# Optimization experiments

Hardware: AMD Instinct MI355X
Metric: run time of the kernel (lower is better)

Reference implementation:

```python
import jax, jax.numpy as jnp
import numpy as np

D_MODEL = 2048
NUM_HEADS = 32
NUM_GROUPS = 8
D_K = D_MODEL // NUM_HEADS          # 64
HPG = NUM_HEADS // NUM_GROUPS       # heads per group = 4
B, S = 2, 2048


def setup_inputs() -> dict:
    key = jax.random.key(0)
    ks = jax.random.split(key, 9)
    w_scale = 0.02
    kv_dim = NUM_GROUPS * D_K
    return {
        "x":  jax.random.normal(ks[0], (B, S, D_MODEL), dtype=jnp.float32),
        "Wq": jax.random.normal(ks[1], (D_MODEL, D_MODEL), dtype=jnp.float32) * w_scale,
        "bq": jnp.zeros((D_MODEL,), dtype=jnp.float32),
        "Wk": jax.random.normal(ks[2], (D_MODEL, kv_dim), dtype=jnp.float32) * w_scale,
        "bk": jnp.zeros((kv_dim,), dtype=jnp.float32),
        "Wv": jax.random.normal(ks[3], (D_MODEL, kv_dim), dtype=jnp.float32) * w_scale,
        "bv": jnp.zeros((kv_dim,), dtype=jnp.float32),
        "Wo": jax.random.normal(ks[4], (D_MODEL, D_MODEL), dtype=jnp.float32) * w_scale,
        "bo": jnp.zeros((D_MODEL,), dtype=jnp.float32),
    }


def reference(x, Wq, bq, Wk, bk, Wv, bv, Wo, bo):
    b, s, _ = x.shape
    # projections (torch Linear math: x @ W^T + b, here weights stored as (in,out))
    Q = (x @ Wq + bq).reshape(b, s, NUM_HEADS, D_K).transpose(0, 2, 1, 3)   # [B,H,S,dk]
    Kg = (x @ Wk + bk).reshape(b, s, NUM_GROUPS, D_K).transpose(0, 2, 1, 3)  # [B,G,S,dk]
    Vg = (x @ Wv + bv).reshape(b, s, NUM_GROUPS, D_K).transpose(0, 2, 1, 3)
    # repeat_interleave K/V over head dim to full head count
    K = jnp.repeat(Kg, HPG, axis=1)  # [B,H,S,dk]
    V = jnp.repeat(Vg, HPG, axis=1)
    scores = jnp.einsum("bhqd,bhkd->bhqk", Q, K) / np.sqrt(D_K).astype(np.float32)
    attn = jax.nn.softmax(scores, axis=-1)
    out = jnp.einsum("bhqk,bhkd->bhqd", attn, V)               # [B,H,S,dk]
    out = out.transpose(0, 2, 1, 3).reshape(b, s, D_MODEL)
    out = out @ Wo + bo
    # module returns grouped K,V cache: K[:, ::HPG] == Kg
    return out, (Kg, Vg)
```

## Files before the change

kernel.cpp:

```cpp
#include <hip/hip_runtime.h>
#include <hip/hip_bf16.h>
#include <stdint.h>

#define S_LEN 2048
#define DM    2048
#define NH    32
#define NG    8
#define DK    64
#define BATCH 2
#define MROWS (BATCH*S_LEN)
#define NQKV  3072
#define SSCALE 0.18033688f

typedef __bf16 bf16x8 __attribute__((ext_vector_type(8)));
typedef short  s16x8  __attribute__((ext_vector_type(8)));
typedef float  f32x4  __attribute__((ext_vector_type(4)));
typedef unsigned int u32x4 __attribute__((ext_vector_type(4)));

__device__ __forceinline__ unsigned short f2b(float f) {
    unsigned int x = __float_as_uint(f);
    unsigned int r = (x + 0x7fffu + ((x >> 16) & 1u)) >> 16;
    return (unsigned short)r;
}
__device__ __forceinline__ bf16x8 ld8(const unsigned short* p) {
    return *(const bf16x8*)p;
}
__device__ __forceinline__ s16x8 cvt8(const float* p) {
    f32x4 a = *(const f32x4*)p;
    f32x4 b = *(const f32x4*)(p + 4);
    s16x8 o;
#pragma unroll
    for (int j = 0; j < 4; j++) { o[j] = (short)f2b(a[j]); o[4 + j] = (short)f2b(b[j]); }
    return o;
}
__device__ __forceinline__ void gl_lds(const unsigned short* g, unsigned short* l) {
    __builtin_amdgcn_global_load_lds(
        (const __attribute__((address_space(1))) unsigned int*)g,
        (__attribute__((address_space(3))) unsigned int*)l, 16, 0, 0);
}
__device__ __forceinline__ void wait_vm4() {
    asm volatile("s_waitcnt vmcnt(4)" ::: "memory");
}
__device__ __forceinline__ void wait_vm0() {
    asm volatile("s_waitcnt vmcnt(0)" ::: "memory");
}
__device__ __forceinline__ void bar() {
    __builtin_amdgcn_sched_barrier(0);
    __builtin_amdgcn_s_barrier();
    __builtin_amdgcn_sched_barrier(0);
}

#define TCVT 4096
#define TQ   4096
#define TK   1024
#define TV   1024
#define TO   4096
#define TB   12
#define NPREP (TCVT+TQ+TK+TV+TO+TB)
__global__ __launch_bounds__(256) void prep_fused(
    const float* __restrict__ x,
    const float* __restrict__ Wq, const float* __restrict__ Wk,
    const float* __restrict__ Wv, const float* __restrict__ Wo,
    const float* __restrict__ bq, const float* __restrict__ bk,
    const float* __restrict__ bv,
    unsigned short* __restrict__ xb,
    unsigned short* __restrict__ WqkvT, unsigned short* __restrict__ WoT,
    float* __restrict__ bqkv) {
    __shared__ float t[32][33];
    int bid = blockIdx.x;
    const int tx = threadIdx.x, ty = threadIdx.y;
    const int flat = ty * 32 + tx;
    if (bid < TCVT) {
        size_t id = (size_t)bid * 256 + flat;
        *(s16x8*)&xb[id * 8] = cvt8(x + id * 8);
        return;
    }
    bid -= TCVT;
    const float* in; unsigned short* out; int C, bx, by;
    if (bid < TQ) { in = Wq; out = WqkvT; C = DM; bx = bid & 63; by = bid >> 6; }
    else if ((bid -= TQ) < TK) { in = Wk; out = WqkvT + (size_t)2048 * DM; C = 512; bx = bid & 15; by = bid >> 4; }
    else if ((bid -= TK) < TV) { in = Wv; out = WqkvT + (size_t)2560 * DM; C = 512; bx = bid & 15; by = bid >> 4; }
    else if ((bid -= TV) < TO) { in = Wo; out = WoT; C = DM; bx = bid & 63; by = bid >> 6; }
    else {
        int i = (bid - TO) * 256 + flat;
        if (i < 2048) bqkv[i] = bq[i];
        else if (i < 2560) bqkv[i] = bk[i - 2048];
        else if (i < 3072) bqkv[i] = bv[i - 2560];
        return;
    }
    const int R = DM;
    int c0 = bx * 32, r0 = by * 32;
#pragma unroll
    for (int i = 0; i < 4; i++)
        t[ty + i * 8][tx] = in[(size_t)(r0 + ty + i * 8) * C + c0 + tx];
    __syncthreads();
#pragma unroll
    for (int i = 0; i < 4; i++)
        out[(size_t)(c0 + ty + i * 8) * R + r0 + tx] = f2b(t[tx][ty + i * 8]);
}

__device__ __forceinline__ void xcd_remap(int gx, int* bx, int* by) {
    int nwg = gx * (int)gridDim.y;
    int flat = (int)blockIdx.y * gx + (int)blockIdx.x;
    int wgid = (flat & 7) * (nwg >> 3) + (flat >> 3);
    *bx = wgid % gx;
    *by = wgid / gx;
}

__global__ __launch_bounds__(256, 3) void gemm_qkv(const unsigned short* __restrict__ A,
                                                const unsigned short* __restrict__ Bt,
                                                const float* __restrict__ bias,
                                                unsigned short* __restrict__ Qb,
                                                float* __restrict__ Kg, float* __restrict__ Vg,
                                                unsigned short* __restrict__ Kb,
                                                unsigned short* __restrict__ Vtb) {
    __shared__ alignas(16) unsigned short As[3][128 * 32];
    __shared__ alignas(16) unsigned short Bs[3][128 * 32];
    const int K = DM;
    const int tid = threadIdx.x;
    int bx, by;
    xcd_remap(NQKV / 128, &bx, &by);
    const int n0 = bx * 128, m0 = by * 128;
    const int w = tid >> 6, lane = tid & 63;
    const int ln15 = lane & 15, quad = lane >> 4;
    const int wm = (w >> 1) * 64, wn = (w & 1) * 64;
    const int xq = (quad ^ ((ln15 >> 1) & 3)) * 8;
    f32x4 acc[4][4] = {};

#define GSTAGE(k0v, buf) do {                                                    \
    _Pragma("unroll")                                                            \
    for (int i = 0; i < 2; ++i) {                                                \
        int s = w * 128 + i * 64 + lane;             \
        int r = s >> 2, cb = (s & 3) ^ ((r >> 1) & 3);                           \
        gl_lds(&A[(size_t)(m0 + r) * K + (k0v) + cb * 8],                        \
               &As[buf][(w * 128 + i * 64) * 8]);                                \
        gl_lds(&Bt[(size_t)(n0 + r) * K + (k0v) + cb * 8],                       \
               &Bs[buf][(w * 128 + i * 64) * 8]);                                \
    } } while (0)

    GSTAGE(0, 0);
    GSTAGE(32, 1);
    int cur = 0;
    for (int k0 = 0; k0 < K; k0 += 32) {
        if (k0 + 32 < K) wait_vm4(); else wait_vm0();
        bar();
        if (k0 + 64 < K) {
            int nb = cur + 2; if (nb >= 3) nb -= 3;
            GSTAGE(k0 + 64, nb);
        }
        bf16x8 af[4], bfr[4];
#pragma unroll
        for (int mt = 0; mt < 4; mt++)
            af[mt] = ld8(&As[cur][(wm + mt * 16 + ln15) * 32 + xq]);
#pragma unroll
        for (int nt = 0; nt < 4; nt++)
            bfr[nt] = ld8(&Bs[cur][(wn + nt * 16 + ln15) * 32 + xq]);
        __builtin_amdgcn_s_setprio(1);
#pragma unroll
        for (int mt = 0; mt < 4; mt++)
#pragma unroll
            for (int nt = 0; nt < 4; nt++)
                acc[mt][nt] = __builtin_amdgcn_mfma_f32_16x16x32_bf16(af[mt], bfr[nt], acc[mt][nt], 0, 0, 0);
        __builtin_amdgcn_s_setprio(0);
        cur = (cur + 1 == 3) ? 0 : cur + 1;
    }
#undef GSTAGE
#pragma unroll
    for (int nt = 0; nt < 4; nt++) {
        int col = n0 + wn + nt * 16 + ln15;
        float bv = bias[col];
#pragma unroll
        for (int mt = 0; mt < 4; mt++) {
            int row0 = m0 + wm + mt * 16 + quad * 4;
#pragma unroll
            for (int r = 0; r < 4; r++) {
                float val = acc[mt][nt][r] + bv;
                int row = row0 + r;
                int b = row >> 11, s = row & 2047;
                if (col < 2048) {
                    Qb[(size_t)row * DM + col] = f2b(val * SSCALE);
                } else if (col < 2560) {
                    int gc = col - 2048, g = gc >> 6, d = gc & 63;
                    size_t idx = (((size_t)(b * NG + g) * S_LEN + s) << 6) + d;
                    Kg[idx] = val;
                    Kb[idx] = f2b(val);
                } else {
                    int gc = col - 2560, g = gc >> 6, d = gc & 63;
                    Vg[(((size_t)(b * NG + g) * S_LEN + s) << 6) + d] = val;
                    Vtb[((size_t)(b * NG + g) * DK + d) * S_LEN + s] = f2b(val);
                }
            }
        }
    }
}

__global__ __launch_bounds__(256, 3) void gemm_o(const unsigned short* __restrict__ A,
                                              const unsigned short* __restrict__ Bt,
                                              const float* __restrict__ bias,
                                              float* __restrict__ C) {
    __shared__ alignas(16) unsigned short As[3][128 * 32];
    __shared__ alignas(16) unsigned short Bs[3][128 * 32];
    const int K = DM, N = DM;
    const int tid = threadIdx.x;
    int bx, by;
    xcd_remap(DM / 128, &bx, &by);
    const int n0 = bx * 128, m0 = by * 128;
    const int w = tid >> 6, lane = tid & 63;
    const int ln15 = lane & 15, quad = lane >> 4;
    const int wm = (w >> 1) * 64, wn = (w & 1) * 64;
    const int xq = (quad ^ ((ln15 >> 1) & 3)) * 8;
    f32x4 acc[4][4] = {};

#define GSTAGE(k0v, buf) do {                                                    \
    _Pragma("unroll")                                                            \
    for (int i = 0; i < 2; ++i) {                                                \
        int s = w * 128 + i * 64 + lane;                                         \
        int r = s >> 2, cb = (s & 3) ^ ((r >> 1) & 3);                           \
        gl_lds(&A[(size_t)(m0 + r) * K + (k0v) + cb * 8],                        \
               &As[buf][(w * 128 + i * 64) * 8]);                                \
        gl_lds(&Bt[(size_t)(n0 + r) * K + (k0v) + cb * 8],                       \
               &Bs[buf][(w * 128 + i * 64) * 8]);                                \
    } } while (0)

    GSTAGE(0, 0);
    GSTAGE(32, 1);
    int cur = 0;
    for (int k0 = 0; k0 < K; k0 += 32) {
        if (k0 + 32 < K) wait_vm4(); else wait_vm0();
        bar();
        if (k0 + 64 < K) {
            int nb = cur + 2; if (nb >= 3) nb -= 3;
            GSTAGE(k0 + 64, nb);
        }
        bf16x8 af[4], bfr[4];
#pragma unroll
        for (int mt = 0; mt < 4; mt++)
            af[mt] = ld8(&As[cur][(wm + mt * 16 + ln15) * 32 + xq]);
#pragma unroll
        for (int nt = 0; nt < 4; nt++)
            bfr[nt] = ld8(&Bs[cur][(wn + nt * 16 + ln15) * 32 + xq]);
        __builtin_amdgcn_s_setprio(1);
#pragma unroll
        for (int mt = 0; mt < 4; mt++)
#pragma unroll
            for (int nt = 0; nt < 4; nt++)
                acc[mt][nt] = __builtin_amdgcn_mfma_f32_16x16x32_bf16(af[mt], bfr[nt], acc[mt][nt], 0, 0, 0);
        __builtin_amdgcn_s_setprio(0);
        cur = (cur + 1 == 3) ? 0 : cur + 1;
    }
#undef GSTAGE
#pragma unroll
    for (int nt = 0; nt < 4; nt++) {
        int col = n0 + wn + nt * 16 + ln15;
        float bv = bias[col];
#pragma unroll
        for (int mt = 0; mt < 4; mt++) {
            int row0 = m0 + wm + mt * 16 + quad * 4;
#pragma unroll
            for (int r = 0; r < 4; r++)
                C[(size_t)(row0 + r) * N + col] = acc[mt][nt][r] + bv;
        }
    }
}

#define MT 2
__global__ __launch_bounds__(512, 4) void attn_fwd(const unsigned short* __restrict__ Qb,
                                                   const unsigned short* __restrict__ Kb,
                                                   const unsigned short* __restrict__ Vtb,
                                                   unsigned short* __restrict__ AO) {
    __shared__ alignas(16) unsigned short Ks[2][2][64 * 64];
    __shared__ alignas(16) unsigned short Vt[2][2][64 * 64];
    const int b = blockIdx.z, h = blockIdx.y, q0 = blockIdx.x * 256;
    const int g = h >> 2;
    const int tid = threadIdx.x;
    const int w = tid >> 6, lane = tid & 63;
    const int ln15 = lane & 15, quad = lane >> 4;
    const int x7a = (quad ^ (ln15 & 7)) * 8;
    const int x7b = x7a ^ 32;

    bf16x8 aq[MT][2];
#pragma unroll
    for (int mt = 0; mt < MT; mt++) {
        const size_t qrow =
            ((size_t)(b * S_LEN + q0 + w * 32 + mt * 16 + ln15)) * DM + h * DK;
        aq[mt][0] = ld8(&Qb[qrow + quad * 8]);
        aq[mt][1] = ld8(&Qb[qrow + 32 + quad * 8]);
    }

    bf16x8 ones;
#pragma unroll
    for (int j = 0; j < 8; j++) ones[j] = (__bf16)1.0f;

    f32x4 o[MT][4] = {};
    f32x4 l_acc[MT] = {};
    const size_t kvb = ((size_t)(b * NG + g)) * S_LEN * DK;

#define STAGE(k0v, buf) do {                                                     \
    int r = tid >> 3, cb = (tid & 7) ^ (r & 7);                                  \
    _Pragma("unroll")                                                            \
    for (int j = 0; j < 2; j++) {                                                \
        gl_lds(&Kb[kvb + (size_t)((k0v) + j * 64 + r) * DK + cb * 8],            \
               &Ks[buf][j][(w * 64) * 8]);                                       \
        gl_lds(&Vtb[kvb + (size_t)r * S_LEN + (k0v) + j * 64 + cb * 8],          \
               &Vt[buf][j][(w * 64) * 8]);                                       \
    } } while (0)

    STAGE(0, 0);
    wait_vm0();
    __syncthreads();
    int cur = 0;

    for (int k0 = 0; k0 < S_LEN; k0 += 128) {
        if (k0 + 128 < S_LEN) STAGE(k0 + 128, cur ^ 1);

#pragma unroll
        for (int sub = 0; sub < 2; sub++) {
            f32x4 z[MT][4];
            __builtin_amdgcn_s_setprio(1);
#pragma unroll
            for (int nt = 0; nt < 4; nt++) {
                bf16x8 bk0 = ld8(&Ks[cur][sub][(nt * 16 + ln15) * 64 + x7a]);
                bf16x8 bk1 = ld8(&Ks[cur][sub][(nt * 16 + ln15) * 64 + x7b]);
#pragma unroll
                for (int mt = 0; mt < MT; mt++) {
                    f32x4 t = {0.f, 0.f, 0.f, 0.f};
                    t = __builtin_amdgcn_mfma_f32_16x16x32_bf16(bk0, aq[mt][0], t, 0, 0, 0);
                    t = __builtin_amdgcn_mfma_f32_16x16x32_bf16(bk1, aq[mt][1], t, 0, 0, 0);
                    z[mt][nt] = t;
                }
            }
            __builtin_amdgcn_s_setprio(0);

            bf16x8 pa[MT][2];
#pragma unroll
            for (int mt = 0; mt < MT; mt++) {
                unsigned int S[4][2];
#pragma unroll
                for (int nt = 0; nt < 4; nt++) {
                    f32x4 pe;
#pragma unroll
                    for (int r = 0; r < 4; r++)
                        pe[r] = __builtin_amdgcn_exp2f(z[mt][nt][r]);
                    asm("v_cvt_pk_bf16_f32 %0, %1, %2" : "=v"(S[nt][0]) : "v"(pe[0]), "v"(pe[1]));
                    asm("v_cvt_pk_bf16_f32 %0, %1, %2" : "=v"(S[nt][1]) : "v"(pe[2]), "v"(pe[3]));
                }
#pragma unroll
                for (int f = 0; f < 2; f++) {
                    unsigned int wA[2], wB[2];
#pragma unroll
                    for (int p = 0; p < 2; p++) {
                        unsigned int xa = S[2 * f][p], yb = S[2 * f + 1][p];
                        asm("v_permlane32_swap_b32 %0, %1" : "+v"(xa), "+v"(yb));
                        asm("v_permlane16_swap_b32 %0, %1" : "+v"(xa), "+v"(yb));
                        wA[p] = xa; wB[p] = yb;
                    }
                    u32x4 t4;
                    t4[0] = wA[0]; t4[1] = wA[1]; t4[2] = wB[0]; t4[3] = wB[1];
                    pa[mt][f] = __builtin_bit_cast(bf16x8, t4);
                }
            }

            __builtin_amdgcn_s_setprio(1);
#pragma unroll
            for (int nt = 0; nt < 4; nt++) {
                bf16x8 bv0 = ld8(&Vt[cur][sub][(nt * 16 + ln15) * 64 + x7a]);
                bf16x8 bv1 = ld8(&Vt[cur][sub][(nt * 16 + ln15) * 64 + x7b]);
#pragma unroll
                for (int mt = 0; mt < MT; mt++) {
                    f32x4 t = o[mt][nt];
                    t = __builtin_amdgcn_mfma_f32_16x16x32_bf16(pa[mt][0], bv0, t, 0, 0, 0);
                    t = __builtin_amdgcn_mfma_f32_16x16x32_bf16(pa[mt][1], bv1, t, 0, 0, 0);
                    o[mt][nt] = t;
                }
            }
#pragma unroll
            for (int mt = 0; mt < MT; mt++) {
                l_acc[mt] = __builtin_amdgcn_mfma_f32_16x16x32_bf16(pa[mt][0], ones, l_acc[mt], 0, 0, 0);
                l_acc[mt] = __builtin_amdgcn_mfma_f32_16x16x32_bf16(pa[mt][1], ones, l_acc[mt], 0, 0, 0);
            }
            __builtin_amdgcn_s_setprio(0);
        }

        wait_vm0();
        __syncthreads();
        cur ^= 1;
    }
#undef STAGE

#pragma unroll
    for (int mt = 0; mt < MT; mt++) {
#pragma unroll
        for (int r = 0; r < 4; r++) {
            float inv = 1.0f / l_acc[mt][r];
            int q = q0 + w * 32 + mt * 16 + quad * 4 + r;
#pragma unroll
            for (int nt = 0; nt < 4; nt++) {
                int col = h * DK + nt * 16 + ln15;
                *(__bf16*)&AO[((size_t)(b * S_LEN + q)) * DM + col] =
                    (__bf16)(o[mt][nt][r] * inv);
            }
        }
    }
}

extern "C" void kernel_launch(void* const* d_in, const int* in_sizes, int n_in,
                              void* d_out, int out_size, void* d_ws, size_t ws_size,
                              hipStream_t stream) {
    const float* x  = (const float*)d_in[0];
    const float* Wq = (const float*)d_in[1];
    const float* bq = (const float*)d_in[2];
    const float* Wk = (const float*)d_in[3];
    const float* bk = (const float*)d_in[4];
    const float* Wv = (const float*)d_in[5];
    const float* bv = (const float*)d_in[6];
    const float* Wo = (const float*)d_in[7];
    const float* bo = (const float*)d_in[8];

    float* out = (float*)d_out;
    float* Kg  = out + (size_t)MROWS * DM;
    float* Vg  = Kg + (size_t)BATCH * NG * S_LEN * DK;

    unsigned short* Qb = (unsigned short*)d_out;

    unsigned short* ws    = (unsigned short*)d_ws;
    unsigned short* WqkvT = ws;
    unsigned short* WoT   = WqkvT + (size_t)NQKV * DM;
    unsigned short* Kb    = WoT + (size_t)DM * DM;
    unsigned short* Vtb   = Kb + (size_t)BATCH * NG * S_LEN * DK;
    unsigned short* AO    = Vtb + (size_t)BATCH * NG * S_LEN * DK;
    unsigned short* xb    = AO + (size_t)MROWS * DM;
    float*          bqkv  = (float*)(xb + (size_t)MROWS * DM);

    hipLaunchKernelGGL(prep_fused, dim3(NPREP), dim3(32, 8), 0, stream,
                       x, Wq, Wk, Wv, Wo, bq, bk, bv, xb, WqkvT, WoT, bqkv);

    hipLaunchKernelGGL(gemm_qkv, dim3(NQKV / 128, MROWS / 128), dim3(256), 0, stream,
                       xb, WqkvT, bqkv, Qb, Kg, Vg, Kb, Vtb);

    hipLaunchKernelGGL(attn_fwd, dim3(S_LEN / 256, NH, BATCH), dim3(512), 0, stream,
                       Qb, Kb, Vtb, AO);

    hipLaunchKernelGGL(gemm_o, dim3(DM / 128, MROWS / 128), dim3(256), 0, stream,
                       AO, WoT, bo, out);
}
```

Baseline: 305.4 us.

## Use 64-row transpose tiles in prep and double-buffer BK=64 in output GEMM

```diff
diff --git a/kernel.cpp b/kernel.cpp
--- a/kernel.cpp
+++ b/kernel.cpp
@@ -51,10 +51,10 @@
 }
 
 #define TCVT 4096
-#define TQ   4096
-#define TK   1024
-#define TV   1024
-#define TO   4096
+#define TQ   2048
+#define TK   512
+#define TV   512
+#define TO   2048
 #define TB   12
 #define NPREP (TCVT+TQ+TK+TV+TO+TB)
 __global__ __launch_bounds__(256) void prep_fused(
@@ -66,7 +66,7 @@
     unsigned short* __restrict__ xb,
     unsigned short* __restrict__ WqkvT, unsigned short* __restrict__ WoT,
     float* __restrict__ bqkv) {
-    __shared__ float t[32][33];
+    __shared__ float t[32][65];
     int bid = blockIdx.x;
     const int tx = threadIdx.x, ty = threadIdx.y;
     const int flat = ty * 32 + tx;
@@ -88,15 +88,15 @@
         else if (i < 3072) bqkv[i] = bv[i - 2560];
         return;
     }
-    const int R = DM;
-    int c0 = bx * 32, r0 = by * 32;
-#pragma unroll
-    for (int i = 0; i < 4; i++)
-        t[ty + i * 8][tx] = in[(size_t)(r0 + ty + i * 8) * C + c0 + tx];
+    int c0 = bx * 32, r0 = by * 64;
+#pragma unroll
+    for (int i = 0; i < 8; i++)
+        t[tx][ty + i * 8] = in[(size_t)(r0 + ty + i * 8) * C + c0 + tx];
     __syncthreads();
-#pragma unroll
-    for (int i = 0; i < 4; i++)
-        out[(size_t)(c0 + ty + i * 8) * R + r0 + tx] = f2b(t[tx][ty + i * 8]);
+    const int rt = flat & 63, cg = flat >> 6;
+#pragma unroll
+    for (int i = 0; i < 8; i++)
+        out[(size_t)(c0 + cg * 8 + i) * DM + r0 + rt] = f2b(t[cg * 8 + i][rt]);
 }
 
 __device__ __forceinline__ void xcd_remap(int gx, int* bx, int* by) {
@@ -194,12 +194,12 @@
     }
 }
 
-__global__ __launch_bounds__(256, 3) void gemm_o(const unsigned short* __restrict__ A,
+__global__ __launch_bounds__(256, 2) void gemm_o(const unsigned short* __restrict__ A,
                                               const unsigned short* __restrict__ Bt,
                                               const float* __restrict__ bias,
                                               float* __restrict__ C) {
-    __shared__ alignas(16) unsigned short As[3][128 * 32];
-    __shared__ alignas(16) unsigned short Bs[3][128 * 32];
+    __shared__ alignas(16) unsigned short As[2][2][128 * 32];
+    __shared__ alignas(16) unsigned short Bs[2][2][128 * 32];
     const int K = DM, N = DM;
     const int tid = threadIdx.x;
     int bx, by;
@@ -211,44 +211,48 @@
     const int xq = (quad ^ ((ln15 >> 1) & 3)) * 8;
     f32x4 acc[4][4] = {};
 
-#define GSTAGE(k0v, buf) do {                                                    \
+#define GSTAGE64(k0v, buf) do {                                                  \
     _Pragma("unroll")                                                            \
-    for (int i = 0; i < 2; ++i) {                                                \
-        int s = w * 128 + i * 64 + lane;                                         \
-        int r = s >> 2, cb = (s & 3) ^ ((r >> 1) & 3);                           \
-        gl_lds(&A[(size_t)(m0 + r) * K + (k0v) + cb * 8],                        \
-               &As[buf][(w * 128 + i * 64) * 8]);                                \
-        gl_lds(&Bt[(size_t)(n0 + r) * K + (k0v) + cb * 8],                       \
-               &Bs[buf][(w * 128 + i * 64) * 8]);                                \
+    for (int j = 0; j < 2; ++j) {                                                \
+        _Pragma("unroll")                                                        \
+        for (int i = 0; i < 2; ++i) {                                            \
+            int s = w * 128 + i * 64 + lane;                                     \
+            int r = s >> 2, cb = (s & 3) ^ ((r >> 1) & 3);                       \
+            gl_lds(&A[(size_t)(m0 + r) * K + (k0v) + j * 32 + cb * 8],           \
+                   &As[buf][j][(w * 128 + i * 64) * 8]);                         \
+            gl_lds(&Bt[(size_t)(n0 + r) * K + (k0v) + j * 32 + cb * 8],          \
+                   &Bs[buf][j][(w * 128 + i * 64) * 8]);                         \
+        }                                                                        \
     } } while (0)
 
-    GSTAGE(0, 0);
-    GSTAGE(32, 1);
+    GSTAGE64(0, 0);
+    wait_vm0();
+    __syncthreads();
     int cur = 0;
-    for (int k0 = 0; k0 < K; k0 += 32) {
-        if (k0 + 32 < K) wait_vm4(); else wait_vm0();
-        bar();
-        if (k0 + 64 < K) {
-            int nb = cur + 2; if (nb >= 3) nb -= 3;
-            GSTAGE(k0 + 64, nb);
-        }
-        bf16x8 af[4], bfr[4];
-#pragma unroll
-        for (int mt = 0; mt < 4; mt++)
-            af[mt] = ld8(&As[cur][(wm + mt * 16 + ln15) * 32 + xq]);
-#pragma unroll
-        for (int nt = 0; nt < 4; nt++)
-            bfr[nt] = ld8(&Bs[cur][(wn + nt * 16 + ln15) * 32 + xq]);
-        __builtin_amdgcn_s_setprio(1);
-#pragma unroll
-        for (int mt = 0; mt < 4; mt++)
+    for (int k0 = 0; k0 < K; k0 += 64) {
+        if (k0 + 64 < K) GSTAGE64(k0 + 64, cur ^ 1);
+#pragma unroll
+        for (int sub = 0; sub < 2; sub++) {
+            bf16x8 af[4], bfr[4];
+#pragma unroll
+            for (int mt = 0; mt < 4; mt++)
+                af[mt] = ld8(&As[cur][sub][(wm + mt * 16 + ln15) * 32 + xq]);
 #pragma unroll
             for (int nt = 0; nt < 4; nt++)
-                acc[mt][nt] = __builtin_amdgcn_mfma_f32_16x16x32_bf16(af[mt], bfr[nt], acc[mt][nt], 0, 0, 0);
-        __builtin_amdgcn_s_setprio(0);
-        cur = (cur + 1 == 3) ? 0 : cur + 1;
-    }
-#undef GSTAGE
+                bfr[nt] = ld8(&Bs[cur][sub][(wn + nt * 16 + ln15) * 32 + xq]);
+            __builtin_amdgcn_s_setprio(1);
+#pragma unroll
+            for (int mt = 0; mt < 4; mt++)
+#pragma unroll
+                for (int nt = 0; nt < 4; nt++)
+                    acc[mt][nt] = __builtin_amdgcn_mfma_f32_16x16x32_bf16(af[mt], bfr[nt], acc[mt][nt], 0, 0, 0);
+            __builtin_amdgcn_s_setprio(0);
+        }
+        wait_vm0();
+        __syncthreads();
+        cur ^= 1;
+    }
+#undef GSTAGE64
 #pragma unroll
     for (int nt = 0; nt < 4; nt++) {
         int col = n0 + wn + nt * 16 + ln15;
```

New measurement: 307.0 us. No clear change (+0.5%).
